# Kernel tuning notes

Measured on AMD Instinct MI355X. Metric: run time of the kernel, lower is better.

Reference implementation:

```python
import jax, jax.numpy as jnp
import numpy as np

R_MAX = 5.0
AVG_NEIGH = 16.0
F = 64          # hidden scalar channels (hidden_irreps count of 0e)
NB = 8          # num_bessel
LMAX = 2
S = 9           # (LMAX+1)^2 spherical-harmonic components
NE = 10         # num_elements
G = 4           # num_graphs
T = 2           # num_interactions
L_OF_LM = np.array([0, 1, 1, 1, 2, 2, 2, 2, 2])


def spherical_harmonics(u):
    # real SH up to l=2, e3nn 'component' normalization; u: [E,3] unit vectors
    x, y, z = u[:, 0], u[:, 1], u[:, 2]
    s3, s5, s15 = 3.0 ** 0.5, 5.0 ** 0.5, 15.0 ** 0.5
    return jnp.stack([
        jnp.ones_like(x),
        s3 * x, s3 * y, s3 * z,
        s15 * x * y, s15 * y * z, (s5 / 2.0) * (3.0 * z * z - 1.0),
        s15 * x * z, (s15 / 2.0) * (x * x - y * y),
    ], axis=-1)  # [E, 9]


def radial_embedding(r):
    # Bessel basis * polynomial cutoff (p=5), as in MACE RadialEmbeddingBlock
    r_safe = jnp.maximum(r, 1e-6)
    n = jnp.arange(1, NB + 1, dtype=r.dtype)  # [NB]
    bessel = jnp.sqrt(2.0 / R_MAX) * jnp.sin(n[None, :] * jnp.pi * r_safe[:, None] / R_MAX) / r_safe[:, None]
    u = r / R_MAX
    p = 5.0
    f = (1.0 - 0.5 * (p + 1) * (p + 2) * u ** 5 + p * (p + 2) * u ** 6 - 0.5 * p * (p + 1) * u ** 7)
    f = f * (u < 1.0)
    return bessel * f[:, None]  # [E, NB]


def setup_inputs() -> dict:
    key = jax.random.key(0)
    ks = jax.random.split(key, 24)
    N, E = 20000, 320000
    positions = jax.random.normal(ks[0], (N, 3), dtype=jnp.float32) * 5.0
    species = jax.random.randint(ks[1], (N,), 0, NE)
    node_attrs = jax.nn.one_hot(species, NE, dtype=jnp.float32)
    edge_index = jax.random.randint(ks[2], (2, E), 0, N)
    shifts = jnp.zeros((E, 3), dtype=jnp.float32)
    batch = jnp.sort(jax.random.randint(ks[3], (N,), 0, G)).astype(jnp.int32)
    charges = jax.random.normal(ks[4], (N,), dtype=jnp.float32) * 0.1
    sc = 1.0 / np.sqrt(F)
    params = {
        'atomic_energies': jax.random.normal(ks[5], (NE,), dtype=jnp.float32),
        'W_embed': jax.random.normal(ks[6], (NE, F), dtype=jnp.float32),
        'Wr0': jax.random.normal(ks[7], (T, NB, 64), dtype=jnp.float32) / np.sqrt(NB),
        'Wr1': jax.random.normal(ks[8], (T, 64, 64), dtype=jnp.float32) / 8.0,
        'Wr2': jax.random.normal(ks[9], (T, 64, F * (LMAX + 1)), dtype=jnp.float32) / 8.0,
        'Wmix': jax.random.normal(ks[10], (T, LMAX + 1, F, F), dtype=jnp.float32) * sc,
        'Wprod': jax.random.normal(ks[11], (T, NE, F, 3), dtype=jnp.float32) * sc,
        'Wread0': jax.random.normal(ks[12], (F,), dtype=jnp.float32) * sc,
        'Wm1': jax.random.normal(ks[13], (F, 16), dtype=jnp.float32) * sc,
        'wm2': jax.random.normal(ks[14], (16,), dtype=jnp.float32) * 0.25,
        'Wq': jax.random.normal(ks[15], (T, F), dtype=jnp.float32) * sc,
    }
    return dict(positions=positions, node_attrs=node_attrs, shifts=shifts,
                charges=charges, edge_index=edge_index, batch=batch, **params)


def _forward(positions, node_attrs, shifts, charges,
             atomic_energies, W_embed, Wr0, Wr1, Wr2, Wmix, Wprod,
             Wread0, Wm1, wm2, Wq, edge_index, batch):
    N = positions.shape[0]
    src, dst = edge_index[0], edge_index[1]
    # isolated-atom reference energies
    node_e0 = node_attrs @ atomic_energies                       # [N]
    e0 = jax.ops.segment_sum(node_e0, batch, num_segments=G)     # [G]
    # edge geometry
    vec = positions[dst] - positions[src] + shifts               # [E,3]
    lengths = jnp.linalg.norm(vec, axis=-1)                      # [E]
    len_safe = jnp.where(lengths > 1e-6, lengths, 1.0)
    unit = vec / len_safe[:, None]
    edge_attrs = spherical_harmonics(unit)                       # [E,S]
    edge_feats = radial_embedding(lengths)                       # [E,NB]
    # node embedding: scalars only, rest of irreps zero
    node_feats = jnp.zeros((N, F, S), dtype=positions.dtype)
    node_feats = node_feats.at[:, :, 0].set(node_attrs @ W_embed)
    charge_density = charges[:, None] * jnp.ones((1, 1), positions.dtype)  # [N,1] formal charges (l=0)
    lm = jnp.asarray(L_OF_LM)
    energy = e0
    for t in range(T):
        # radial MLP -> per-edge tensor-product weights [E,F,LMAX+1]
        h = jax.nn.silu(edge_feats @ Wr0[t])
        h = jax.nn.silu(h @ Wr1[t])
        w = (h @ Wr2[t]).reshape(-1, F, LMAX + 1)
        wl = w[:, :, lm]                                         # [E,F,S]
        s_src = node_feats[src, :, 0]                            # [E,F] gather
        msg = wl * s_src[:, :, None] * edge_attrs[:, None, :]    # [E,F,S]
        A = jax.ops.segment_sum(msg, dst, num_segments=N) / AVG_NEIGH  # [N,F,S] scatter
        # per-l linear channel mixing
        A = jnp.einsum('nfs,sfg->ngs', A, Wmix[t][lm])
        # symmetric product basis (correlation 3), element-dependent weights
        wp = jnp.einsum('ne,efc->nfc', node_attrs, Wprod[t])     # [N,F,3]
        p1 = A[:, :, 0]                                          # scalar invariant
        p2 = jnp.sum(A * A, axis=-1)                             # norm invariant
        scale = wp[:, :, 0] + wp[:, :, 1] * p1 + wp[:, :, 2] * p2
        new_feats = A * scale[:, :, None]
        if t > 0:
            new_feats = new_feats + node_feats                   # residual self-connection
        node_feats = new_feats
        scal = node_feats[:, :, 0]
        if t == T - 1:
            node_en = jax.nn.silu(scal @ Wm1) @ wm2              # nonlinear readout
        else:
            node_en = scal @ Wread0                              # linear readout
        energy = energy + jax.ops.segment_sum(node_en, batch, num_segments=G)
        charge_density = charge_density + (scal @ Wq[t])[:, None]
    return energy  # [G]


def reference(positions, node_attrs, shifts, charges, edge_index, batch,
              atomic_energies, W_embed, Wr0, Wr1, Wr2, Wmix, Wprod,
              Wread0, Wm1, wm2, Wq):
    return _forward(positions, node_attrs, shifts, charges,
                    atomic_energies, W_embed, Wr0, Wr1, Wr2, Wmix, Wprod,
                    Wread0, Wm1, wm2, Wq, edge_index, batch)
```

## Files before the change

kernel.cpp:

```cpp
#include <hip/hip_runtime.h>
#include <hip/hip_bf16.h>

#define F 64
#define NB 8
#define NE 10
#define GSEG 4
#define EPW 256
#define NTAB 2048

typedef __attribute__((ext_vector_type(8))) short short8v;
typedef __attribute__((ext_vector_type(4))) float float4v;

__device__ __forceinline__ float silu(float x) {
    return x / (1.0f + __expf(-x));
}

__device__ __forceinline__ float bcast(float v, int lane) {
    return __uint_as_float(__builtin_amdgcn_readlane(__float_as_uint(v), lane));
}

__device__ __forceinline__ unsigned short f2bf(float x) {
    unsigned int u = __float_as_uint(x);
    u += 0x7FFFu + ((u >> 16) & 1u);
    return (unsigned short)(u >> 16);
}

__global__ __launch_bounds__(256) void init_and_tables(
    const float* __restrict__ node_attrs, const float* __restrict__ AE,
    const float* __restrict__ W_embed, const int* __restrict__ batch,
    const float* __restrict__ pos,
    float* __restrict__ S0, float* __restrict__ epart,
    int* __restrict__ deg, float4* __restrict__ pos4,
    int* __restrict__ spec, int N, int nodeBlocks,
    const float* __restrict__ Wr0, const float* __restrict__ Wr1,
    const float* __restrict__ Wr2, float* __restrict__ Tab,
    const float* __restrict__ Wmix, unsigned short* __restrict__ Wbt,
    int tabBlocks)
{
    int w = threadIdx.x >> 6, lane = threadIdx.x & 63;

    if (blockIdx.x < (unsigned)nodeBlocks) {
        int n = blockIdx.x * 4 + w;
        if (n >= N) return;
        float sc = 0.0f, e0 = 0.0f;
        int sp = 0;
        #pragma unroll
        for (int e = 0; e < NE; e++) {
            float a = node_attrs[n * NE + e];
            sc = fmaf(a, W_embed[e * F + lane], sc);
            e0 = fmaf(a, AE[e], e0);
            if (a > 0.5f) sp = e;
        }
        S0[(size_t)n * F + lane] = sc;
        if (lane == 0) {
            deg[n] = 0;
            spec[n] = sp;
            pos4[n] = make_float4(pos[n * 3], pos[n * 3 + 1], pos[n * 3 + 2], 0.f);
            atomicAdd(&epart[batch[n] * EPW + (n & (EPW - 1))], e0);
        }
        return;
    }

    if (blockIdx.x >= (unsigned)(nodeBlocks + tabBlocks)) {
        int i = (blockIdx.x - nodeBlocks - tabBlocks) * 256 + threadIdx.x;
        if (i >= 2 * 3 * 4096) return;
        int tl = i >> 12;
        int gf = i & 4095;
        int g = gf >> 6, f = gf & 63;
        Wbt[i] = f2bf(Wmix[(size_t)(tl * 64 + f) * 64 + g] * 0.0625f);
        return;
    }

    const int blocksPerTab = (NTAB + 1 + 3) / 4;
    int bid = blockIdx.x - nodeBlocks;
    int tab = bid / blocksPerTab;
    int eidx = (bid - tab * blocksPerTab) * 4 + w;
    if (eidx > NTAB) return;
    const float* W0 = Wr0 + tab * 512;
    const float* W1 = Wr1 + tab * 4096;
    const float* W2 = Wr2 + tab * 12288;

    float r = (float)eidx * (5.0f / NTAB);
    float rs = fmaxf(r, 1e-6f);
    float s1, c1;
    __sincosf(0.6283185307179586f * rs, &s1, &c1);
    float u = r * 0.2f;
    float u2 = u * u, u4 = u2 * u2, u5 = u4 * u, u6 = u5 * u, u7 = u6 * u;
    float fc = 1.0f - 21.0f * u5 + 35.0f * u6 - 15.0f * u7;
    float pref = 0.6324555320336759f / rs * fc;
    float ef[NB];
    {
        float sp = 0.0f, sc_ = s1, tc = 2.0f * c1;
        #pragma unroll
        for (int k = 0; k < NB; k++) {
            ef[k] = pref * sc_;
            float sn = tc * sc_ - sp;
            sp = sc_; sc_ = sn;
        }
    }

    float a1 = 0.0f;
    #pragma unroll
    for (int k = 0; k < NB; k++) a1 = fmaf(ef[k], W0[k * 64 + lane], a1);
    float h1 = silu(a1);

    float a2 = 0.0f;
    #pragma unroll 8
    for (int k = 0; k < 64; k++)
        a2 = fmaf(bcast(h1, k), W1[k * 64 + lane], a2);
    float h2 = silu(a2);

    float w0 = 0.f, w1 = 0.f, w2 = 0.f;
    #pragma unroll 8
    for (int k = 0; k < 64; k++) {
        float hk = bcast(h2, k);
        const float* wr = W2 + k * 192 + lane * 3;
        w0 = fmaf(hk, wr[0], w0);
        w1 = fmaf(hk, wr[1], w1);
        w2 = fmaf(hk, wr[2], w2);
    }

    float* Trow = Tab + ((size_t)tab * (NTAB + 1) + eidx) * 192;
    Trow[lane] = w0;
    Trow[64 + lane] = w1;
    Trow[128 + lane] = w2;
}

__global__ __launch_bounds__(256) void edge_prep(
    const float4* __restrict__ pos4, const float* __restrict__ shifts,
    const int* __restrict__ EI, int E,
    float4* __restrict__ geoFull, int* __restrict__ deg)
{
    int e = blockIdx.x * 256 + threadIdx.x;
    if (e >= E) return;
    int s = EI[e], d = EI[E + e];
    float4 pd = pos4[d], ps = pos4[s];
    float vx = pd.x - ps.x + shifts[e * 3 + 0];
    float vy = pd.y - ps.y + shifts[e * 3 + 1];
    float vz = pd.z - ps.z + shifts[e * 3 + 2];
    float len = sqrtf(vx * vx + vy * vy + vz * vz);
    float ls = (len > 1e-6f) ? len : 1.0f;
    float inv = 1.0f / ls;
    geoFull[e] = make_float4(vx * inv, vy * inv, vz * inv, len);
    if (len < 5.0f) atomicAdd(&deg[d], 1);
}

__global__ __launch_bounds__(256) void alloc_start(
    const int* __restrict__ deg, int* __restrict__ start,
    int* __restrict__ cursor, int* __restrict__ total, int N)
{
    __shared__ int wsum[4];
    __shared__ int gbase;
    int t = threadIdx.x;
    int n = blockIdx.x * 256 + t;
    int lane = t & 63, w = t >> 6;
    int v = (n < N) ? deg[n] : 0;
    int inc = v;
    #pragma unroll
    for (int off = 1; off < 64; off <<= 1) {
        int u = __shfl_up(inc, off);
        if (lane >= off) inc += u;
    }
    if (lane == 63) wsum[w] = inc;
    __syncthreads();
    if (t == 0) {
        int s0 = wsum[0], s1 = wsum[1], s2 = wsum[2], s3 = wsum[3];
        int bs = s0 + s1 + s2 + s3;
        wsum[0] = 0; wsum[1] = s0; wsum[2] = s0 + s1; wsum[3] = s0 + s1 + s2;
        gbase = atomicAdd(total, bs);
    }
    __syncthreads();
    if (n < N) {
        int st = gbase + wsum[w] + (inc - v);
        start[n] = st;
        cursor[n] = st;
    }
}

__global__ __launch_bounds__(256) void csr_fill(
    const float4* __restrict__ geoFull, const int* __restrict__ EI, int E,
    int* __restrict__ cursor,
    float4* __restrict__ geoS, int* __restrict__ srcS, int EB)
{
    int e = blockIdx.x * 256 + threadIdx.x;
    if (e >= E) return;
    float4 gv = geoFull[e];
    if (gv.w < 5.0f) {
        int d = EI[E + e];
        int p = atomicAdd(&cursor[d], 1);
        if (p < EB) {
            geoS[p] = gv;
            srcS[p] = EI[e];
        }
    }
}

template <int PHASE>
__global__ __launch_bounds__(1024) void gather_mix(
    const float4* __restrict__ geoS, const int* __restrict__ srcS,
    const float* __restrict__ Tab,
    const int* __restrict__ start, const int* __restrict__ deg,
    const unsigned short* __restrict__ Wbt,
    const float* __restrict__ Wprodt, const int* __restrict__ spec,
    const int* __restrict__ batch,
    const float* __restrict__ Wread0, const float* __restrict__ Wm1,
    const float* __restrict__ wm2,
    const float* __restrict__ Sin, float* __restrict__ Sout,
    float* __restrict__ epart, int N)
{
    __shared__ unsigned short Abf[9 * 1088];
    __shared__ float Osh[9 * 1088];

    int t = threadIdx.x;
    int lane = t & 63, w = t >> 6;
    int l15 = lane & 15, quad = lane >> 4;
    int n0 = blockIdx.x * 16;
    int n = n0 + w;
    int g = lane;

    float am0 = 0.f, am1 = 0.f, am2_ = 0.f, am3 = 0.f, am4 = 0.f,
          am5 = 0.f, am6 = 0.f, am7 = 0.f, am8 = 0.f;
    if (n < N) {
        int st = start[n], dg = deg[n];
        const float s3 = 1.7320508075688772f;
        const float s5h = 1.1180339887498948f;
        const float s15 = 3.8729833462074170f;
        const float s15h = 1.9364916731037085f;
        for (int i = st; i < st + dg; i++) {
            float4 gv = geoS[i];
            int srcn = srcS[i];
            float sv = Sin[(size_t)srcn * F + g];
            float scaled = gv.w * (NTAB / 5.0f);
            int idx = (int)scaled;
            float fr = scaled - (float)idx;
            const float* T0 = Tab + (size_t)idx * 192;
            float wa = T0[g],        wb = T0[192 + g];
            float wc = T0[64 + g],   wd = T0[256 + g];
            float we = T0[128 + g],  wf_ = T0[320 + g];
            float w0 = fmaf(fr, wb - wa, wa);
            float w1 = fmaf(fr, wd - wc, wc);
            float w2 = fmaf(fr, wf_ - we, we);

            float ux = gv.x, uy = gv.y, uz = gv.z;
            float m0 = w0 * sv, m1 = w1 * sv, m2 = w2 * sv;
            am0 += m0;
            am1 = fmaf(m1, s3 * ux, am1);
            am2_ = fmaf(m1, s3 * uy, am2_);
            am3 = fmaf(m1, s3 * uz, am3);
            am4 = fmaf(m2, s15 * ux * uy, am4);
            am5 = fmaf(m2, s15 * uy * uz, am5);
            am6 = fmaf(m2, s5h * (3.0f * uz * uz - 1.0f), am6);
            am7 = fmaf(m2, s15 * ux * uz, am7);
            am8 = fmaf(m2, s15h * (ux * ux - uy * uy), am8);
        }
    }
    int arow = w * 68 + g;
    Abf[0 * 1088 + arow] = f2bf(am0);
    Abf[1 * 1088 + arow] = f2bf(am1);
    Abf[2 * 1088 + arow] = f2bf(am2_);
    Abf[3 * 1088 + arow] = f2bf(am3);
    Abf[4 * 1088 + arow] = f2bf(am4);
    Abf[5 * 1088 + arow] = f2bf(am5);
    Abf[6 * 1088 + arow] = f2bf(am6);
    Abf[7 * 1088 + arow] = f2bf(am7);
    Abf[8 * 1088 + arow] = f2bf(am8);
    __syncthreads();

    if (w < 9) {
        int s = w;
        int l = (s == 0) ? 0 : ((s < 4) ? 1 : 2);
        const unsigned short* Bp = Wbt + l * 4096 + (size_t)l15 * 64;
        const unsigned short* Ar = &Abf[s * 1088 + l15 * 68];
        short8v a0 = *(const short8v*)(Ar + quad * 8);
        short8v a1 = *(const short8v*)(Ar + 32 + quad * 8);
        #pragma unroll
        for (int nt = 0; nt < 4; nt++) {
            short8v b0 = *(const short8v*)(Bp + nt * 1024 + quad * 8);
            short8v b1 = *(const short8v*)(Bp + nt * 1024 + 32 + quad * 8);
            float4v acc = {0.f, 0.f, 0.f, 0.f};
            acc = __builtin_amdgcn_mfma_f32_16x16x32_bf16(a0, b0, acc, 0, 0, 0);
            acc = __builtin_amdgcn_mfma_f32_16x16x32_bf16(a1, b1, acc, 0, 0, 0);
            #pragma unroll
            for (int r = 0; r < 4; r++)
                Osh[s * 1088 + (quad * 4 + r) * 68 + nt * 16 + l15] = acc[r];
        }
    }
    __syncthreads();

    if (n >= N) return;
    int b = batch[n];
    float bb[9];
    #pragma unroll
    for (int s = 0; s < 9; s++) bb[s] = Osh[s * 1088 + w * 68 + lane];

    int sp = spec[n];
    const float* W = Wprodt + (sp * F + lane) * 3;
    float wp0 = W[0], wp1 = W[1], wp2 = W[2];

    float p1 = bb[0];
    float p2 = 0.f;
    #pragma unroll
    for (int s = 0; s < 9; s++) p2 = fmaf(bb[s], bb[s], p2);
    float scale = wp0 + wp1 * p1 + wp2 * p2;
    float sc0 = bb[0] * scale;

    if (PHASE == 0) {
        Sout[(size_t)n * F + lane] = sc0;
        float vv = sc0 * Wread0[lane];
        #pragma unroll
        for (int off = 32; off > 0; off >>= 1) vv += __shfl_xor(vv, off);
        if (lane == 0) atomicAdd(&epart[b * EPW + (n & (EPW - 1))], vv);
    } else {
        sc0 += Sin[(size_t)n * F + lane];
        int gi = lane & 15;
        float acc = 0.0f;
        #pragma unroll 8
        for (int k = 0; k < 64; k++)
            acc = fmaf(bcast(sc0, k), Wm1[k * 16 + gi], acc);
        float vv = (lane < 16) ? silu(acc) * wm2[gi] : 0.0f;
        #pragma unroll
        for (int off = 32; off > 0; off >>= 1) vv += __shfl_xor(vv, off);
        if (lane == 0) atomicAdd(&epart[b * EPW + (n & (EPW - 1))], vv);
    }
}

__global__ __launch_bounds__(256) void reduce_energy(
    const float* __restrict__ epart, float* __restrict__ out)
{
    int t = threadIdx.x;
    __shared__ float ps[GSEG][4];
    for (int b = 0; b < GSEG; b++) {
        float v = epart[b * EPW + t];
        #pragma unroll
        for (int off = 32; off > 0; off >>= 1) v += __shfl_xor(v, off);
        if ((t & 63) == 0) ps[b][t >> 6] = v;
    }
    __syncthreads();
    if (t < GSEG) out[t] = ps[t][0] + ps[t][1] + ps[t][2] + ps[t][3];
}

extern "C" void kernel_launch(void* const* d_in, const int* in_sizes, int n_in,
                              void* d_out, int out_size, void* d_ws, size_t ws_size,
                              hipStream_t stream) {
    const float* positions  = (const float*)d_in[0];
    const float* node_attrs = (const float*)d_in[1];
    const float* shifts     = (const float*)d_in[2];
    const int*   edge_index = (const int*)d_in[4];
    const int*   batch      = (const int*)d_in[5];
    const float* AE         = (const float*)d_in[6];
    const float* W_embed    = (const float*)d_in[7];
    const float* Wr0        = (const float*)d_in[8];
    const float* Wr1        = (const float*)d_in[9];
    const float* Wr2        = (const float*)d_in[10];
    const float* Wmix       = (const float*)d_in[11];
    const float* Wprod      = (const float*)d_in[12];
    const float* Wread0     = (const float*)d_in[13];
    const float* Wm1        = (const float*)d_in[14];
    const float* wm2        = (const float*)d_in[15];

    int N = in_sizes[0] / 3;
    int E = in_sizes[4] / 2;
    int EB = E / 8;
    float* out = (float*)d_out;

    char* ws = (char*)d_ws;
    size_t off = 0;
    auto alignup = [](size_t v) { return (v + 255) & ~(size_t)255; };
    float4* geoFull = (float4*)(ws + off); off = alignup(off + (size_t)E * sizeof(float4));
    float4* geoS  = (float4*)(ws + off); off = alignup(off + (size_t)EB * sizeof(float4));
    float4* pos4  = (float4*)(ws + off); off = alignup(off + (size_t)N * sizeof(float4));
    float*  S0    = (float*)(ws + off);  off = alignup(off + (size_t)N * F * sizeof(float));
    float*  S1    = (float*)(ws + off);  off = alignup(off + (size_t)N * F * sizeof(float));
    int*    srcS  = (int*)(ws + off);    off = alignup(off + (size_t)EB * sizeof(int));
    int*    deg   = (int*)(ws + off);    off = alignup(off + (size_t)N * sizeof(int));
    int*    start = (int*)(ws + off);    off = alignup(off + (size_t)N * sizeof(int));
    int*    cursor= (int*)(ws + off);    off = alignup(off + (size_t)N * sizeof(int));
    int*    spec  = (int*)(ws + off);    off = alignup(off + (size_t)N * sizeof(int));
    float*  epart = (float*)(ws + off);
    int*    total = (int*)(ws + off + GSEG * EPW * sizeof(float));
    off = alignup(off + GSEG * EPW * sizeof(float) + 128);
    float*  Tab   = (float*)(ws + off);
    off = alignup(off + (size_t)2 * (NTAB + 1) * 192 * sizeof(float));
    unsigned short* Wbt = (unsigned short*)(ws + off);
    off = alignup(off + (size_t)2 * 3 * 4096 * sizeof(unsigned short));

    hipMemsetAsync(epart, 0, GSEG * EPW * sizeof(float) + 128, stream);

    int nodeBlocks4 = (N + 3) / 4;
    int nodeBlocks256 = (N + 255) / 256;
    int edgeBlocks = (E + 255) / 256;
    int tabBlocks = 2 * ((NTAB + 1 + 3) / 4);
    int wbBlocks = (2 * 3 * 4096 + 255) / 256;
    int gmBlocks = (N + 15) / 16;
    size_t tabStride = (size_t)(NTAB + 1) * 192;

    init_and_tables<<<nodeBlocks4 + tabBlocks + wbBlocks, 256, 0, stream>>>(
        node_attrs, AE, W_embed, batch, positions,
        S0, epart, deg, pos4, spec, N, nodeBlocks4,
        Wr0, Wr1, Wr2, Tab, Wmix, Wbt, tabBlocks);
    edge_prep<<<edgeBlocks, 256, 0, stream>>>(pos4, shifts, edge_index, E,
                                              geoFull, deg);
    alloc_start<<<nodeBlocks256, 256, 0, stream>>>(deg, start, cursor, total, N);
    csr_fill<<<edgeBlocks, 256, 0, stream>>>(geoFull, edge_index, E,
                                             cursor, geoS, srcS, EB);

    gather_mix<0><<<gmBlocks, 1024, 0, stream>>>(geoS, srcS, Tab, start, deg,
                                                 Wbt, Wprod, spec, batch,
                                                 Wread0, Wm1, wm2,
                                                 S0, S1, epart, N);
    gather_mix<1><<<gmBlocks, 1024, 0, stream>>>(geoS, srcS, Tab + tabStride,
                                                 start, deg,
                                                 Wbt + 3 * 4096,
                                                 Wprod + NE * F * 3, spec, batch,
                                                 Wread0, Wm1, wm2,
                                                 S1, S1, epart, N);

    reduce_energy<<<1, 256, 0, stream>>>(epart, out);
}
```

Baseline: 217.0 us.

## Halve gather_mix block size, two nodes per wave, alias bf16 A tile into Osh

Each gather_mix block now runs 8 waves instead of 16, and each wave gathers edges for two destination nodes one after the other. The bf16 A tile is stored inside the Osh float buffer instead of a separate shared array, which cuts LDS per block. batch, spec, the residual and the Wprod weights are prefetched before the gather loops, and the MFMA stage loops so 8 waves cover the 9 SH components. The aim is more resident blocks per CU and less LDS pressure, in exchange for serialized per-wave gathers and less parallelism across nodes within a block.

```diff
diff --git a/kernel.cpp b/kernel.cpp
--- a/kernel.cpp
+++ b/kernel.cpp
@@ -196,7 +196,7 @@
 }
 
 template <int PHASE>
-__global__ __launch_bounds__(1024) void gather_mix(
+__global__ __launch_bounds__(512) void gather_mix(
     const float4* __restrict__ geoS, const int* __restrict__ srcS,
     const float* __restrict__ Tab,
     const int* __restrict__ start, const int* __restrict__ deg,
@@ -208,69 +208,83 @@
     const float* __restrict__ Sin, float* __restrict__ Sout,
     float* __restrict__ epart, int N)
 {
-    __shared__ unsigned short Abf[9 * 1088];
     __shared__ float Osh[9 * 1088];
 
     int t = threadIdx.x;
     int lane = t & 63, w = t >> 6;
     int l15 = lane & 15, quad = lane >> 4;
     int n0 = blockIdx.x * 16;
-    int n = n0 + w;
-    int g = lane;
-
-    float am0 = 0.f, am1 = 0.f, am2_ = 0.f, am3 = 0.f, am4 = 0.f,
-          am5 = 0.f, am6 = 0.f, am7 = 0.f, am8 = 0.f;
-    if (n < N) {
-        int st = start[n], dg = deg[n];
-        const float s3 = 1.7320508075688772f;
-        const float s5h = 1.1180339887498948f;
-        const float s15 = 3.8729833462074170f;
-        const float s15h = 1.9364916731037085f;
-        for (int i = st; i < st + dg; i++) {
-            float4 gv = geoS[i];
-            int srcn = srcS[i];
-            float sv = Sin[(size_t)srcn * F + g];
-            float scaled = gv.w * (NTAB / 5.0f);
-            int idx = (int)scaled;
-            float fr = scaled - (float)idx;
-            const float* T0 = Tab + (size_t)idx * 192;
-            float wa = T0[g],        wb = T0[192 + g];
-            float wc = T0[64 + g],   wd = T0[256 + g];
-            float we = T0[128 + g],  wf_ = T0[320 + g];
-            float w0 = fmaf(fr, wb - wa, wa);
-            float w1 = fmaf(fr, wd - wc, wc);
-            float w2 = fmaf(fr, wf_ - we, we);
-
-            float ux = gv.x, uy = gv.y, uz = gv.z;
-            float m0 = w0 * sv, m1 = w1 * sv, m2 = w2 * sv;
-            am0 += m0;
-            am1 = fmaf(m1, s3 * ux, am1);
-            am2_ = fmaf(m1, s3 * uy, am2_);
-            am3 = fmaf(m1, s3 * uz, am3);
-            am4 = fmaf(m2, s15 * ux * uy, am4);
-            am5 = fmaf(m2, s15 * uy * uz, am5);
-            am6 = fmaf(m2, s5h * (3.0f * uz * uz - 1.0f), am6);
-            am7 = fmaf(m2, s15 * ux * uz, am7);
-            am8 = fmaf(m2, s15h * (ux * ux - uy * uy), am8);
-        }
-    }
-    int arow = w * 68 + g;
-    Abf[0 * 1088 + arow] = f2bf(am0);
-    Abf[1 * 1088 + arow] = f2bf(am1);
-    Abf[2 * 1088 + arow] = f2bf(am2_);
-    Abf[3 * 1088 + arow] = f2bf(am3);
-    Abf[4 * 1088 + arow] = f2bf(am4);
-    Abf[5 * 1088 + arow] = f2bf(am5);
-    Abf[6 * 1088 + arow] = f2bf(am6);
-    Abf[7 * 1088 + arow] = f2bf(am7);
-    Abf[8 * 1088 + arow] = f2bf(am8);
+
+    int nn[2] = {n0 + w, n0 + w + 8};
+    int b[2] = {0, 0}, sp[2] = {0, 0};
+    float resid[2] = {0.f, 0.f};
+    #pragma unroll
+    for (int j = 0; j < 2; j++) {
+        if (nn[j] < N) {
+            b[j] = batch[nn[j]];
+            sp[j] = spec[nn[j]];
+            if (PHASE == 1) resid[j] = Sin[(size_t)nn[j] * F + lane];
+        }
+    }
+
+    const float s3 = 1.7320508075688772f;
+    const float s5h = 1.1180339887498948f;
+    const float s15 = 3.8729833462074170f;
+    const float s15h = 1.9364916731037085f;
+    #pragma unroll
+    for (int j = 0; j < 2; j++) {
+        int n = nn[j];
+        int v = w + j * 8;
+        float am[9] = {0.f, 0.f, 0.f, 0.f, 0.f, 0.f, 0.f, 0.f, 0.f};
+        if (n < N) {
+            int st = start[n], iend = st + deg[n];
+            for (int i = st; i < iend; i++) {
+                float4 gv = geoS[i];
+                int srcn = srcS[i];
+                float sv = Sin[(size_t)srcn * F + lane];
+                float scaled = gv.w * (NTAB / 5.0f);
+                int idx = (int)scaled;
+                float fr = scaled - (float)idx;
+                const float* T0 = Tab + (size_t)idx * 192;
+                float wa = T0[lane],       wb = T0[192 + lane];
+                float wc = T0[64 + lane],  wd = T0[256 + lane];
+                float we = T0[128 + lane], wf_ = T0[320 + lane];
+                float w0 = fmaf(fr, wb - wa, wa);
+                float w1 = fmaf(fr, wd - wc, wc);
+                float w2 = fmaf(fr, wf_ - we, we);
+                float ux = gv.x, uy = gv.y, uz = gv.z;
+                float m0 = w0 * sv, m1 = w1 * sv, m2 = w2 * sv;
+                am[0] += m0;
+                am[1] = fmaf(m1, s3 * ux, am[1]);
+                am[2] = fmaf(m1, s3 * uy, am[2]);
+                am[3] = fmaf(m1, s3 * uz, am[3]);
+                am[4] = fmaf(m2, s15 * ux * uy, am[4]);
+                am[5] = fmaf(m2, s15 * uy * uz, am[5]);
+                am[6] = fmaf(m2, s5h * (3.0f * uz * uz - 1.0f), am[6]);
+                am[7] = fmaf(m2, s15 * ux * uz, am[7]);
+                am[8] = fmaf(m2, s15h * (ux * ux - uy * uy), am[8]);
+            }
+        }
+        #pragma unroll
+        for (int s = 0; s < 9; s++)
+            ((unsigned short*)(Osh + s * 1088))[v * 68 + lane] = f2bf(am[s]);
+    }
+
+    float wp[2][3] = {{0.f, 0.f, 0.f}, {0.f, 0.f, 0.f}};
+    #pragma unroll
+    for (int j = 0; j < 2; j++) {
+        if (nn[j] < N) {
+            const float* W = Wprodt + (sp[j] * F + lane) * 3;
+            wp[j][0] = W[0]; wp[j][1] = W[1]; wp[j][2] = W[2];
+        }
+    }
     __syncthreads();
 
-    if (w < 9) {
-        int s = w;
+    for (int s = w; s < 9; s += 8) {
         int l = (s == 0) ? 0 : ((s < 4) ? 1 : 2);
         const unsigned short* Bp = Wbt + l * 4096 + (size_t)l15 * 64;
-        const unsigned short* Ar = &Abf[s * 1088 + l15 * 68];
+        const unsigned short* Ar =
+            (const unsigned short*)(Osh + s * 1088) + l15 * 68;
         short8v a0 = *(const short8v*)(Ar + quad * 8);
         short8v a1 = *(const short8v*)(Ar + 32 + quad * 8);
         #pragma unroll
@@ -287,40 +301,40 @@
     }
     __syncthreads();
 
-    if (n >= N) return;
-    int b = batch[n];
-    float bb[9];
-    #pragma unroll
-    for (int s = 0; s < 9; s++) bb[s] = Osh[s * 1088 + w * 68 + lane];
-
-    int sp = spec[n];
-    const float* W = Wprodt + (sp * F + lane) * 3;
-    float wp0 = W[0], wp1 = W[1], wp2 = W[2];
-
-    float p1 = bb[0];
-    float p2 = 0.f;
-    #pragma unroll
-    for (int s = 0; s < 9; s++) p2 = fmaf(bb[s], bb[s], p2);
-    float scale = wp0 + wp1 * p1 + wp2 * p2;
-    float sc0 = bb[0] * scale;
-
-    if (PHASE == 0) {
-        Sout[(size_t)n * F + lane] = sc0;
-        float vv = sc0 * Wread0[lane];
-        #pragma unroll
-        for (int off = 32; off > 0; off >>= 1) vv += __shfl_xor(vv, off);
-        if (lane == 0) atomicAdd(&epart[b * EPW + (n & (EPW - 1))], vv);
-    } else {
-        sc0 += Sin[(size_t)n * F + lane];
-        int gi = lane & 15;
-        float acc = 0.0f;
-        #pragma unroll 8
-        for (int k = 0; k < 64; k++)
-            acc = fmaf(bcast(sc0, k), Wm1[k * 16 + gi], acc);
-        float vv = (lane < 16) ? silu(acc) * wm2[gi] : 0.0f;
-        #pragma unroll
-        for (int off = 32; off > 0; off >>= 1) vv += __shfl_xor(vv, off);
-        if (lane == 0) atomicAdd(&epart[b * EPW + (n & (EPW - 1))], vv);
+    #pragma unroll
+    for (int j = 0; j < 2; j++) {
+        int n = nn[j];
+        if (n >= N) continue;
+        int v = w + j * 8;
+        float bb[9];
+        #pragma unroll
+        for (int s = 0; s < 9; s++) bb[s] = Osh[s * 1088 + v * 68 + lane];
+
+        float p1 = bb[0];
+        float p2 = 0.f;
+        #pragma unroll
+        for (int s = 0; s < 9; s++) p2 = fmaf(bb[s], bb[s], p2);
+        float scale = wp[j][0] + wp[j][1] * p1 + wp[j][2] * p2;
+        float sc0 = bb[0] * scale;
+
+        if (PHASE == 0) {
+            Sout[(size_t)n * F + lane] = sc0;
+            float vv = sc0 * Wread0[lane];
+            #pragma unroll
+            for (int off = 32; off > 0; off >>= 1) vv += __shfl_xor(vv, off);
+            if (lane == 0) atomicAdd(&epart[b[j] * EPW + (n & (EPW - 1))], vv);
+        } else {
+            sc0 += resid[j];
+            int gi = lane & 15;
+            float acc = 0.0f;
+            #pragma unroll 8
+            for (int k = 0; k < 64; k++)
+                acc = fmaf(bcast(sc0, k), Wm1[k * 16 + gi], acc);
+            float vv = (lane < 16) ? silu(acc) * wm2[gi] : 0.0f;
+            #pragma unroll
+            for (int off = 32; off > 0; off >>= 1) vv += __shfl_xor(vv, off);
+            if (lane == 0) atomicAdd(&epart[b[j] * EPW + (n & (EPW - 1))], vv);
+        }
     }
 }
 
@@ -404,16 +418,16 @@
     csr_fill<<<edgeBlocks, 256, 0, stream>>>(geoFull, edge_index, E,
                                              cursor, geoS, srcS, EB);
 
-    gather_mix<0><<<gmBlocks, 1024, 0, stream>>>(geoS, srcS, Tab, start, deg,
-                                                 Wbt, Wprod, spec, batch,
-                                                 Wread0, Wm1, wm2,
-                                                 S0, S1, epart, N);
-    gather_mix<1><<<gmBlocks, 1024, 0, stream>>>(geoS, srcS, Tab + tabStride,
-                                                 start, deg,
-                                                 Wbt + 3 * 4096,
-                                                 Wprod + NE * F * 3, spec, batch,
-                                                 Wread0, Wm1, wm2,
-                                                 S1, S1, epart, N);
+    gather_mix<0><<<gmBlocks, 512, 0, stream>>>(geoS, srcS, Tab, start, deg,
+                                                Wbt, Wprod, spec, batch,
+                                                Wread0, Wm1, wm2,
+                                                S0, S1, epart, N);
+    gather_mix<1><<<gmBlocks, 512, 0, stream>>>(geoS, srcS, Tab + tabStride,
+                                                start, deg,
+                                                Wbt + 3 * 4096,
+                                                Wprod + NE * F * 3, spec, batch,
+                                                Wread0, Wm1, wm2,
+                                                S1, S1, epart, N);
 
     reduce_energy<<<1, 256, 0, stream>>>(epart, out);
 }
```

After: 211.5 us, median of 2. 2.5% less time.
